# Kernel tuning notes

Hardware: AMD Instinct MI355X
Metric: run time of the kernel (lower is better)

## Reference

```python
import jax, jax.numpy as jnp
import numpy as np

D_MODEL = 1024
N_HEADS = 16
D_HEAD = D_MODEL // N_HEADS
SCALE = D_HEAD ** -0.5


def setup_inputs() -> dict:
    key = jax.random.key(0)
    ks = jax.random.split(key, 9)
    s = 0.02
    x = jax.random.normal(ks[0], (2, 2048, D_MODEL), dtype=jnp.float32)
    Wq = jax.random.normal(ks[1], (D_MODEL, D_MODEL), dtype=jnp.float32) * s
    Wk = jax.random.normal(ks[2], (D_MODEL, D_MODEL), dtype=jnp.float32) * s
    Wv = jax.random.normal(ks[3], (D_MODEL, D_MODEL), dtype=jnp.float32) * s
    Wo = jax.random.normal(ks[4], (D_MODEL, D_MODEL), dtype=jnp.float32) * s
    bq = jax.random.normal(ks[5], (D_MODEL,), dtype=jnp.float32) * s
    bk = jax.random.normal(ks[6], (D_MODEL,), dtype=jnp.float32) * s
    bv = jax.random.normal(ks[7], (D_MODEL,), dtype=jnp.float32) * s
    bo = jax.random.normal(ks[8], (D_MODEL,), dtype=jnp.float32) * s
    return {"x": x, "Wq": Wq, "bq": bq, "Wk": Wk, "bk": bk,
            "Wv": Wv, "bv": bv, "Wo": Wo, "bo": bo}


def reference(x, Wq, bq, Wk, bk, Wv, bv, Wo, bo):
    B, S, _ = x.shape
    # torch nn.Linear: y = x @ W.T + b
    def proj(W, b):
        h = jnp.einsum('bsd,ed->bse', x, W) + b
        return h.reshape(B, S, N_HEADS, D_HEAD).transpose(0, 2, 1, 3)  # [B,H,S,Dh]
    Q = proj(Wq, bq)
    K = proj(Wk, bk)
    V = proj(Wv, bv)
    # chunked QK^T softmax over full K == full attention (no mask, dropout=0)
    scores = jnp.einsum('bhqd,bhkd->bhqk', Q, K) * SCALE  # [B,H,S,S]
    attn = jax.nn.softmax(scores, axis=-1)
    out = jnp.einsum('bhqk,bhkd->bhqd', attn, V)
    out = out.transpose(0, 2, 1, 3).reshape(B, S, D_MODEL)
    return jnp.einsum('bsd,ed->bse', out, Wo) + bo
```

## Files before the change

kernel.cpp:

```cpp
#include <hip/hip_runtime.h>
#include <cstdint>
#include <cstddef>


typedef unsigned short u16;
typedef unsigned int u32;
typedef __bf16 bf16x8 __attribute__((ext_vector_type(8)));
typedef float f32x4 __attribute__((ext_vector_type(4)));

#define GLOAD_LDS16(gp, lp)                                                            \
  __builtin_amdgcn_global_load_lds((const __attribute__((address_space(1))) void*)(gp),\
                                   (__attribute__((address_space(3))) void*)(lp),      \
                                   16, 0, 0)

__device__ __forceinline__ u16 f2bf(float f) {
  unsigned u = __builtin_bit_cast(unsigned, f);
  u = u + 0x7fffu + ((u >> 16) & 1u);
  return (u16)(u >> 16);
}

__device__ __forceinline__ u32 pack_bf2(float a, float b) {
  u32 ua = __builtin_bit_cast(u32, a) + 0x8000u;
  u32 ub = __builtin_bit_cast(u32, b) + 0x8000u;
  return __builtin_amdgcn_perm(ub, ua, 0x07060302u);
}

#define QSCALE 0.1803368801111204f

__global__ void cvt_all(const float* __restrict__ x,
                        const float* __restrict__ wq, const float* __restrict__ wk,
                        const float* __restrict__ wv, const float* __restrict__ wo,
                        u16* __restrict__ xb, u16* __restrict__ wqb,
                        u16* __restrict__ wkb, u16* __restrict__ wvb,
                        u16* __restrict__ wob) {
  int bx = blockIdx.x;
  const float* s; u16* d; int off;
  if (bx < 2048)      { s = x;  d = xb;  off = bx; }
  else if (bx < 2560) { s = wq; d = wqb; off = bx - 2048; }
  else if (bx < 3072) { s = wk; d = wkb; off = bx - 2560; }
  else if (bx < 3584) { s = wv; d = wvb; off = bx - 3072; }
  else                { s = wo; d = wob; off = bx - 3584; }
  int i = off * 2048 + threadIdx.x * 8;
  float4 a = *(const float4*)(s + i);
  float4 b = *(const float4*)(s + i + 4);
  uint4 o;
  o.x = f2bf(a.x) | ((u32)f2bf(a.y) << 16);
  o.y = f2bf(a.z) | ((u32)f2bf(a.w) << 16);
  o.z = f2bf(b.x) | ((u32)f2bf(b.y) << 16);
  o.w = f2bf(b.z) | ((u32)f2bf(b.w) << 16);
  *(uint4*)(d + i) = o;
}

template <int MODE, int BM>
__global__ __launch_bounds__(256, 3) void gemm_mfma(
    const u16* __restrict__ A,
    const u16* __restrict__ W0, const u16* __restrict__ W1, const u16* __restrict__ W2,
    const float* __restrict__ b0, const float* __restrict__ b1, const float* __restrict__ b2,
    u16* __restrict__ o0, u16* __restrict__ o1, u16* __restrict__ o2,
    float* __restrict__ oF)
{
  constexpr int MF = BM / 32;
  constexpr int AG = BM / 32;

  __shared__ __align__(16) u16 As[BM * 64];
  __shared__ __align__(16) u16 Bs[128 * 64];

  const int tid = threadIdx.x;
  const int w = tid >> 6, l = tid & 63;
  const int lane = l & 15, quad = l >> 4;
  const int wm = w >> 1, wn = w & 1;
  const int m0 = blockIdx.y * BM;
  const int n0g = blockIdx.x * 128;

  const int src = (MODE == 0) ? (n0g >> 10) : 0;
  const u16* Wsel = (MODE == 0) ? (src == 0 ? W0 : (src == 1 ? W1 : W2)) : W0;
  const float* bsel = (MODE == 0) ? (src == 0 ? b0 : (src == 1 ? b1 : b2)) : b0;
  const int n_base = (MODE == 0) ? (n0g & 1023) : n0g;

  const int c8 = ((l & 7) ^ (l >> 3)) * 8;
  const int lrow = l >> 3;

  f32x4 acc[MF][4] = {};

  for (int kt = 0; kt < 1024; kt += 64) {
    __syncthreads();
    const u16* Ag = A + (size_t)m0 * 1024 + kt;
    const u16* Bg = Wsel + (size_t)n_base * 1024 + kt;
    #pragma unroll
    for (int i = 0; i < AG; ++i) {
      int rr = w * (8 * AG) + i * 8;
      GLOAD_LDS16(Ag + (size_t)(rr + lrow) * 1024 + c8, As + rr * 64);
    }
    #pragma unroll
    for (int i = 0; i < 4; ++i) {
      int rr = w * 32 + i * 8;
      GLOAD_LDS16(Bg + (size_t)(rr + lrow) * 1024 + c8, Bs + rr * 64);
    }
    __syncthreads();

    bf16x8 af[MF][2], bf[4][2];
    #pragma unroll
    for (int mf = 0; mf < MF; ++mf)
      #pragma unroll
      for (int ks = 0; ks < 2; ++ks)
        af[mf][ks] = *(const bf16x8*)((const char*)As +
            (wm * (BM / 2) + mf * 16 + lane) * 128 + (((ks * 4 + quad) ^ (lane & 7)) * 16));
    #pragma unroll
    for (int nf = 0; nf < 4; ++nf)
      #pragma unroll
      for (int ks = 0; ks < 2; ++ks)
        bf[nf][ks] = *(const bf16x8*)((const char*)Bs +
            (wn * 64 + nf * 16 + lane) * 128 + (((ks * 4 + quad) ^ (lane & 7)) * 16));
    #pragma unroll
    for (int ks = 0; ks < 2; ++ks)
      #pragma unroll
      for (int mf = 0; mf < MF; ++mf)
        #pragma unroll
        for (int nf = 0; nf < 4; ++nf)
          acc[mf][nf] = __builtin_amdgcn_mfma_f32_16x16x32_bf16(
              af[mf][ks], bf[nf][ks], acc[mf][nf], 0, 0, 0);
  }

  float bb[4];
  #pragma unroll
  for (int nf = 0; nf < 4; ++nf) bb[nf] = bsel[n_base + wn * 64 + nf * 16 + lane];

  u16* osel = (MODE == 0) ? (src == 0 ? o0 : (src == 1 ? o1 : o2)) : o0;

  #pragma unroll
  for (int mf = 0; mf < MF; ++mf) {
    int mb = m0 + wm * (BM / 2) + mf * 16 + quad * 4;
    #pragma unroll
    for (int nf = 0; nf < 4; ++nf) {
      int n_l = wn * 64 + nf * 16 + lane;
      if (MODE == 0 && src != 1) {
        float sc = (src == 0) ? QSCALE : 1.0f;
        float v0 = (acc[mf][nf][0] + bb[nf]) * sc;
        float v1 = (acc[mf][nf][1] + bb[nf]) * sc;
        float v2 = (acc[mf][nf][2] + bb[nf]) * sc;
        float v3 = (acc[mf][nf][3] + bb[nf]) * sc;
        int bi = mb >> 11, s = mb & 2047;
        int n_in = n_base + n_l;
        int h = n_in >> 6, dh = n_in & 63;
        uint2 pk = make_uint2(pack_bf2(v0, v1), pack_bf2(v2, v3));
        *(uint2*)(osel + (((size_t)(bi * 16 + h) * 64 + dh) * 2048 + s)) = pk;
      } else {
        #pragma unroll
        for (int r = 0; r < 4; ++r) {
          float v = acc[mf][nf][r] + bb[nf];
          int m = mb + r;
          if (MODE == 0) {
            int bi = m >> 11, s = m & 2047;
            int n_in = n_base + n_l;
            int h = n_in >> 6, dh = n_in & 63;
            osel[(((size_t)(bi * 16 + h) * 2048 + s) << 6) + dh] = f2bf(v);
          } else {
            oF[(size_t)m * 1024 + n0g + n_l] = v;
          }
        }
      }
    }
  }
}

union SMemU {
  struct {
    u16 K[3][64 * 64];
    u16 V[3][64 * 64];
  } m;
  struct {
    float O[4][32 * 64];
    float L[4][32];
  } f;
};

__global__ __launch_bounds__(512, 4) void attn_mfma(
    const u16* __restrict__ Qg_, const u16* __restrict__ Kg_,
    const u16* __restrict__ VTg_, u16* __restrict__ Og)
{
  __shared__ __align__(16) SMemU sm;

  const int tid = threadIdx.x;
  const int w = tid >> 6, l = tid & 63;
  const int lane = l & 15, quad = l >> 4;
  const int g = w >> 1;
  const int kh = w & 1;
  const int bh = blockIdx.y;
  const int q0 = blockIdx.x * 128;

  const u16* QTg = Qg_ + (size_t)bh * 64 * 2048;
  const u16* Kg  = Kg_ + (size_t)bh * 2048 * 64;
  const u16* VTg = VTg_ + (size_t)bh * 64 * 2048;

  const int c8 = ((l & 7) ^ (l >> 3)) * 8;
  const int lrow = l >> 3;
  const int rr = w * 8;

  const int qcol = q0 + g * 32 + lane;
  bf16x8 bq[2][2];
  #pragma unroll
  for (int qf = 0; qf < 2; ++qf)
    #pragma unroll
    for (int ks = 0; ks < 2; ++ks) {
      bf16x8 v;
      #pragma unroll
      for (int j = 0; j < 8; ++j)
        v[j] = __builtin_bit_cast(__bf16,
            QTg[(size_t)(ks * 32 + quad * 8 + j) * 2048 + qcol + qf * 16]);
      bq[qf][ks] = v;
    }

  GLOAD_LDS16(Kg + (size_t)(rr + lrow) * 64 + c8, sm.m.K[0] + rr * 64);
  GLOAD_LDS16(VTg + (size_t)(rr + lrow) * 2048 + c8, sm.m.V[0] + rr * 64);
  GLOAD_LDS16(Kg + (size_t)(64 + rr + lrow) * 64 + c8, sm.m.K[1] + rr * 64);
  GLOAD_LDS16(VTg + (size_t)(rr + lrow) * 2048 + 64 + c8, sm.m.V[1] + rr * 64);

  f32x4 oa[2][4] = {};
  float lsum[2] = {0.f, 0.f};
  int cur = 0;

  for (int kt = 0; kt < 32; ++kt) {
    if (kt < 31) asm volatile("s_waitcnt vmcnt(2)" ::: "memory");
    else         asm volatile("s_waitcnt vmcnt(0)" ::: "memory");
    __builtin_amdgcn_s_barrier();
    asm volatile("" ::: "memory");

    if (kt < 30) {
      int pf = (cur == 0) ? 2 : cur - 1;
      GLOAD_LDS16(Kg + (size_t)((kt + 2) * 64 + rr + lrow) * 64 + c8,
                  sm.m.K[pf] + rr * 64);
      GLOAD_LDS16(VTg + (size_t)(rr + lrow) * 2048 + (kt + 2) * 64 + c8,
                  sm.m.V[pf] + rr * 64);
    }

    f32x4 sa[2][2] = {};
    #pragma unroll
    for (int ks = 0; ks < 2; ++ks) {
      bf16x8 ak[2];
      #pragma unroll
      for (int kf = 0; kf < 2; ++kf)
        ak[kf] = *(const bf16x8*)((const char*)sm.m.K[cur] +
            (kh * 32 + kf * 16 + lane) * 128 + (((ks * 4 + quad) ^ (lane & 7)) * 16));
      #pragma unroll
      for (int kf = 0; kf < 2; ++kf)
        #pragma unroll
        for (int qf = 0; qf < 2; ++qf)
          sa[kf][qf] = __builtin_amdgcn_mfma_f32_16x16x32_bf16(
              ak[kf], bq[qf][ks], sa[kf][qf], 0, 0, 0);
    }

    bf16x8 ap[2];
    #pragma unroll
    for (int qf = 0; qf < 2; ++qf) {
      float x0 = __builtin_amdgcn_exp2f(sa[0][qf][0]);
      float x1 = __builtin_amdgcn_exp2f(sa[0][qf][1]);
      float x2 = __builtin_amdgcn_exp2f(sa[0][qf][2]);
      float x3 = __builtin_amdgcn_exp2f(sa[0][qf][3]);
      float y0 = __builtin_amdgcn_exp2f(sa[1][qf][0]);
      float y1 = __builtin_amdgcn_exp2f(sa[1][qf][1]);
      float y2 = __builtin_amdgcn_exp2f(sa[1][qf][2]);
      float y3 = __builtin_amdgcn_exp2f(sa[1][qf][3]);
      lsum[qf] += ((x0 + x1) + (x2 + x3)) + ((y0 + y1) + (y2 + y3));
      u32 X0 = pack_bf2(x0, x1), X1 = pack_bf2(x2, x3);
      u32 Y0 = pack_bf2(y0, y1), Y1 = pack_bf2(y2, y3);
      asm("v_permlane32_swap_b32 %0, %1" : "+v"(X0), "+v"(Y0));
      asm("v_permlane16_swap_b32 %0, %1" : "+v"(X0), "+v"(Y0));
      asm("v_permlane32_swap_b32 %0, %1" : "+v"(X1), "+v"(Y1));
      asm("v_permlane16_swap_b32 %0, %1" : "+v"(X1), "+v"(Y1));
      uint4 d4 = make_uint4(X0, X1, Y0, Y1);
      ap[qf] = __builtin_bit_cast(bf16x8, d4);
    }

    {
      bf16x8 bv[4];
      #pragma unroll
      for (int df = 0; df < 4; ++df)
        bv[df] = *(const bf16x8*)((const char*)sm.m.V[cur] +
            (df * 16 + lane) * 128 + (((kh * 4 + quad) ^ (lane & 7)) * 16));
      #pragma unroll
      for (int qf = 0; qf < 2; ++qf)
        #pragma unroll
        for (int df = 0; df < 4; ++df)
          oa[qf][df] = __builtin_amdgcn_mfma_f32_16x16x32_bf16(
              ap[qf], bv[df], oa[qf][df], 0, 0, 0);
    }

    cur = (cur == 2) ? 0 : cur + 1;
  }

  #pragma unroll
  for (int qf = 0; qf < 2; ++qf) {
    lsum[qf] += __shfl_xor(lsum[qf], 16);
    lsum[qf] += __shfl_xor(lsum[qf], 32);
  }

  __syncthreads();
  if (kh == 1) {
    #pragma unroll
    for (int qf = 0; qf < 2; ++qf)
      #pragma unroll
      for (int df = 0; df < 4; ++df)
        #pragma unroll
        for (int r = 0; r < 4; ++r)
          sm.f.O[g][(qf * 16 + quad * 4 + r) * 64 + df * 16 + lane] = oa[qf][df][r];
    if (l < 16) {
      sm.f.L[g][l] = lsum[0];
      sm.f.L[g][16 + l] = lsum[1];
    }
  }
  __syncthreads();
  if (kh == 0) {
    const int b = bh >> 4, hh = bh & 15;
    u16* Ob = Og + ((size_t)b * 2048 + q0 + g * 32) * 1024 + hh * 64;
    float ltot[2];
    #pragma unroll
    for (int qf = 0; qf < 2; ++qf)
      ltot[qf] = lsum[qf] + sm.f.L[g][qf * 16 + lane];
    #pragma unroll
    for (int qf = 0; qf < 2; ++qf)
      #pragma unroll
      for (int r = 0; r < 4; ++r) {
        float inv = 1.0f / __shfl(ltot[qf], quad * 4 + r, 16);
        int qrow = qf * 16 + quad * 4 + r;
        #pragma unroll
        for (int df = 0; df < 4; ++df) {
          float v = oa[qf][df][r] + sm.f.O[g][qrow * 64 + df * 16 + lane];
          Ob[(size_t)qrow * 1024 + df * 16 + lane] = f2bf(v * inv);
        }
      }
  }
}

extern "C" void kernel_launch(void* const* d_in, const int* in_sizes, int n_in,
                              void* d_out, int out_size, void* d_ws, size_t ws_size,
                              hipStream_t stream)
{
  (void)in_sizes; (void)n_in; (void)out_size; (void)ws_size;
  const float* x  = (const float*)d_in[0];
  const float* Wq = (const float*)d_in[1];
  const float* bq = (const float*)d_in[2];
  const float* Wk = (const float*)d_in[3];
  const float* bk = (const float*)d_in[4];
  const float* Wv = (const float*)d_in[5];
  const float* bv = (const float*)d_in[6];
  const float* Wo = (const float*)d_in[7];
  const float* bo = (const float*)d_in[8];
  float* y = (float*)d_out;

  const size_t NM = (size_t)4096 * 1024;
  u16* xb  = (u16*)d_ws;
  u16* wqb = xb + NM;
  u16* wkb = wqb + 1024 * 1024;
  u16* wvb = wkb + 1024 * 1024;
  u16* wob = wvb + 1024 * 1024;
  u16* Qb  = wob + 1024 * 1024;
  u16* Kb  = Qb + NM;
  u16* VTb = Kb + NM;
  u16* AOb = VTb + NM;

  cvt_all<<<4096, 256, 0, stream>>>(x, Wq, Wk, Wv, Wo, xb, wqb, wkb, wvb, wob);

  gemm_mfma<0, 128><<<dim3(24, 32), 256, 0, stream>>>(
      xb, wqb, wkb, wvb, bq, bk, bv, Qb, Kb, VTb, nullptr);

  attn_mfma<<<dim3(16, 32), 512, 0, stream>>>(Qb, Kb, VTb, AOb);

  gemm_mfma<1, 64><<<dim3(8, 64), 256, 0, stream>>>(
      AOb, wob, nullptr, nullptr, bo, nullptr, nullptr,
      nullptr, nullptr, nullptr, y);
}
```

Measured before the change: 184.1 us.

## Fuse fp32-to-bf16 conversion into GEMM loads and remap block order for XCD locality

Removes the separate cvt_all conversion kernel. The GEMMs now read fp32 x and weights directly, convert them with v_cvt_pk_bf16_f32 and store the result to LDS through registers instead of global_load_lds. Block indices in the GEMM and attention kernels are remapped so that consecutive blocks in each group of eight go to the same tile region, which is meant to improve L2 locality per XCD. In exchange the GEMMs read twice the bytes per tile and repeat the conversion in every block that shares a tile. The async direct-to-LDS path is lost for fp32 operands, and the hardware cvt may round differently from the old software rounding.

```diff
diff --git a/kernel.cpp b/kernel.cpp
--- a/kernel.cpp
+++ b/kernel.cpp
@@ -19,6 +19,12 @@
   return (u16)(u >> 16);
 }
 
+__device__ __forceinline__ u32 cvtpk(float a, float b) {
+  u32 r;
+  asm("v_cvt_pk_bf16_f32 %0, %1, %2" : "=v"(r) : "v"(a), "v"(b));
+  return r;
+}
+
 __device__ __forceinline__ u32 pack_bf2(float a, float b) {
   u32 ua = __builtin_bit_cast(u32, a) + 0x8000u;
   u32 ub = __builtin_bit_cast(u32, b) + 0x8000u;
@@ -27,40 +33,20 @@
 
 #define QSCALE 0.1803368801111204f
 
-__global__ void cvt_all(const float* __restrict__ x,
-                        const float* __restrict__ wq, const float* __restrict__ wk,
-                        const float* __restrict__ wv, const float* __restrict__ wo,
-                        u16* __restrict__ xb, u16* __restrict__ wqb,
-                        u16* __restrict__ wkb, u16* __restrict__ wvb,
-                        u16* __restrict__ wob) {
-  int bx = blockIdx.x;
-  const float* s; u16* d; int off;
-  if (bx < 2048)      { s = x;  d = xb;  off = bx; }
-  else if (bx < 2560) { s = wq; d = wqb; off = bx - 2048; }
-  else if (bx < 3072) { s = wk; d = wkb; off = bx - 2560; }
-  else if (bx < 3584) { s = wv; d = wvb; off = bx - 3072; }
-  else                { s = wo; d = wob; off = bx - 3584; }
-  int i = off * 2048 + threadIdx.x * 8;
-  float4 a = *(const float4*)(s + i);
-  float4 b = *(const float4*)(s + i + 4);
-  uint4 o;
-  o.x = f2bf(a.x) | ((u32)f2bf(a.y) << 16);
-  o.y = f2bf(a.z) | ((u32)f2bf(a.w) << 16);
-  o.z = f2bf(b.x) | ((u32)f2bf(b.y) << 16);
-  o.w = f2bf(b.z) | ((u32)f2bf(b.w) << 16);
-  *(uint4*)(d + i) = o;
-}
-
 template <int MODE, int BM>
 __global__ __launch_bounds__(256, 3) void gemm_mfma(
-    const u16* __restrict__ A,
-    const u16* __restrict__ W0, const u16* __restrict__ W1, const u16* __restrict__ W2,
-    const float* __restrict__ b0, const float* __restrict__ b1, const float* __restrict__ b2,
+    const float* __restrict__ Af, const u16* __restrict__ Ab,
+    const float* __restrict__ W0, const float* __restrict__ W1,
+    const float* __restrict__ W2,
+    const float* __restrict__ b0, const float* __restrict__ b1,
+    const float* __restrict__ b2,
     u16* __restrict__ o0, u16* __restrict__ o1, u16* __restrict__ o2,
     float* __restrict__ oF)
 {
   constexpr int MF = BM / 32;
   constexpr int AG = BM / 32;
+  constexpr int NY = (MODE == 0) ? 32 : 64;
+  constexpr int TOT = (MODE == 0) ? 24 * 32 : 8 * 64;
 
   __shared__ __align__(16) u16 As[BM * 64];
   __shared__ __align__(16) u16 Bs[128 * 64];
@@ -69,11 +55,14 @@
   const int w = tid >> 6, l = tid & 63;
   const int lane = l & 15, quad = l >> 4;
   const int wm = w >> 1, wn = w & 1;
-  const int m0 = blockIdx.y * BM;
-  const int n0g = blockIdx.x * 128;
+
+  const int idb = blockIdx.y * gridDim.x + blockIdx.x;
+  const int lid = (idb & 7) * (TOT >> 3) + (idb >> 3);
+  const int m0 = (lid % NY) * BM;
+  const int n0g = (lid / NY) * 128;
 
   const int src = (MODE == 0) ? (n0g >> 10) : 0;
-  const u16* Wsel = (MODE == 0) ? (src == 0 ? W0 : (src == 1 ? W1 : W2)) : W0;
+  const float* Wsel = (MODE == 0) ? (src == 0 ? W0 : (src == 1 ? W1 : W2)) : W0;
   const float* bsel = (MODE == 0) ? (src == 0 ? b0 : (src == 1 ? b1 : b2)) : b0;
   const int n_base = (MODE == 0) ? (n0g & 1023) : n0g;
 
@@ -84,17 +73,38 @@
 
   for (int kt = 0; kt < 1024; kt += 64) {
     __syncthreads();
-    const u16* Ag = A + (size_t)m0 * 1024 + kt;
-    const u16* Bg = Wsel + (size_t)n_base * 1024 + kt;
-    #pragma unroll
-    for (int i = 0; i < AG; ++i) {
-      int rr = w * (8 * AG) + i * 8;
-      GLOAD_LDS16(Ag + (size_t)(rr + lrow) * 1024 + c8, As + rr * 64);
-    }
-    #pragma unroll
-    for (int i = 0; i < 4; ++i) {
-      int rr = w * 32 + i * 8;
-      GLOAD_LDS16(Bg + (size_t)(rr + lrow) * 1024 + c8, Bs + rr * 64);
+    if (MODE == 0) {
+      const float* Ag = Af + (size_t)m0 * 1024 + kt;
+      #pragma unroll
+      for (int i = 0; i < AG; ++i) {
+        int rr = w * (8 * AG) + i * 8;
+        const float* s4 = Ag + (size_t)(rr + lrow) * 1024 + c8;
+        float4 a0 = *(const float4*)(s4);
+        float4 a1 = *(const float4*)(s4 + 4);
+        *(uint4*)((char*)As + rr * 128 + l * 16) =
+            make_uint4(cvtpk(a0.x, a0.y), cvtpk(a0.z, a0.w),
+                       cvtpk(a1.x, a1.y), cvtpk(a1.z, a1.w));
+      }
+    } else {
+      const u16* Ag = Ab + (size_t)m0 * 1024 + kt;
+      #pragma unroll
+      for (int i = 0; i < AG; ++i) {
+        int rr = w * (8 * AG) + i * 8;
+        GLOAD_LDS16(Ag + (size_t)(rr + lrow) * 1024 + c8, As + rr * 64);
+      }
+    }
+    {
+      const float* Bg = Wsel + (size_t)n_base * 1024 + kt;
+      #pragma unroll
+      for (int i = 0; i < 4; ++i) {
+        int rr = w * 32 + i * 8;
+        const float* s4 = Bg + (size_t)(rr + lrow) * 1024 + c8;
+        float4 a0 = *(const float4*)(s4);
+        float4 a1 = *(const float4*)(s4 + 4);
+        *(uint4*)((char*)Bs + rr * 128 + l * 16) =
+            make_uint4(cvtpk(a0.x, a0.y), cvtpk(a0.z, a0.w),
+                       cvtpk(a1.x, a1.y), cvtpk(a1.z, a1.w));
+      }
     }
     __syncthreads();
 
@@ -185,8 +195,11 @@
   const int lane = l & 15, quad = l >> 4;
   const int g = w >> 1;
   const int kh = w & 1;
-  const int bh = blockIdx.y;
-  const int q0 = blockIdx.x * 128;
+
+  const int idb = blockIdx.y * 16 + blockIdx.x;
+  const int lid = (idb & 7) * 64 + (idb >> 3);
+  const int bh = lid >> 4;
+  const int q0 = (lid & 15) * 128;
 
   const u16* QTg = Qg_ + (size_t)bh * 64 * 2048;
   const u16* Kg  = Kg_ + (size_t)bh * 2048 * 64;
@@ -348,24 +361,17 @@
   float* y = (float*)d_out;
 
   const size_t NM = (size_t)4096 * 1024;
-  u16* xb  = (u16*)d_ws;
-  u16* wqb = xb + NM;
-  u16* wkb = wqb + 1024 * 1024;
-  u16* wvb = wkb + 1024 * 1024;
-  u16* wob = wvb + 1024 * 1024;
-  u16* Qb  = wob + 1024 * 1024;
+  u16* Qb  = (u16*)d_ws;
   u16* Kb  = Qb + NM;
   u16* VTb = Kb + NM;
   u16* AOb = VTb + NM;
 
-  cvt_all<<<4096, 256, 0, stream>>>(x, Wq, Wk, Wv, Wo, xb, wqb, wkb, wvb, wob);
-
   gemm_mfma<0, 128><<<dim3(24, 32), 256, 0, stream>>>(
-      xb, wqb, wkb, wvb, bq, bk, bv, Qb, Kb, VTb, nullptr);
+      x, nullptr, Wq, Wk, Wv, bq, bk, bv, Qb, Kb, VTb, nullptr);
 
   attn_mfma<<<dim3(16, 32), 512, 0, stream>>>(Qb, Kb, VTb, AOb);
 
   gemm_mfma<1, 64><<<dim3(8, 64), 256, 0, stream>>>(
-      AOb, wob, nullptr, nullptr, bo, nullptr, nullptr,
+      nullptr, AOb, Wo, nullptr, nullptr, bo, nullptr, nullptr,
       nullptr, nullptr, nullptr, y);
 }
```

Measured after the change: 206.3 us. 12.1% more time.

## Remap block IDs for XCD-aware locality and shrink output GEMM tile

Applied to the files above, without the earlier changes.

Block indices in both GEMMs and the attention kernel are remapped so that consecutive blocks dispatched round-robin to each of the 8 XCDs share the same weight columns or the same head, which should improve L2 reuse. The output projection GEMM now uses a 64x64 tile with twice as many blocks and a higher occupancy hint, giving the 256 CUs more parallelism. The smaller tile lowers per-block reuse and adds more redundant A loads.

```diff
diff --git a/kernel.cpp b/kernel.cpp
--- a/kernel.cpp
+++ b/kernel.cpp
@@ -51,8 +51,8 @@
   *(uint4*)(d + i) = o;
 }
 
-template <int MODE, int BM>
-__global__ __launch_bounds__(256, 3) void gemm_mfma(
+template <int MODE, int BM, int BN>
+__global__ __launch_bounds__(256, MODE == 0 ? 3 : 4) void gemm_mfma(
     const u16* __restrict__ A,
     const u16* __restrict__ W0, const u16* __restrict__ W1, const u16* __restrict__ W2,
     const float* __restrict__ b0, const float* __restrict__ b1, const float* __restrict__ b2,
@@ -60,17 +60,24 @@
     float* __restrict__ oF)
 {
   constexpr int MF = BM / 32;
+  constexpr int NF = BN / 32;
   constexpr int AG = BM / 32;
+  constexpr int BG = BN / 32;
+  constexpr int NY = (MODE == 0) ? 32 : 64;
+  constexpr int TOT = (MODE == 0) ? 24 * 32 : 16 * 64;
 
   __shared__ __align__(16) u16 As[BM * 64];
-  __shared__ __align__(16) u16 Bs[128 * 64];
+  __shared__ __align__(16) u16 Bs[BN * 64];
 
   const int tid = threadIdx.x;
   const int w = tid >> 6, l = tid & 63;
   const int lane = l & 15, quad = l >> 4;
   const int wm = w >> 1, wn = w & 1;
-  const int m0 = blockIdx.y * BM;
-  const int n0g = blockIdx.x * 128;
+
+  const int idb = blockIdx.y * gridDim.x + blockIdx.x;
+  const int lid = (idb & 7) * (TOT >> 3) + (idb >> 3);
+  const int m0 = (lid % NY) * BM;
+  const int n0g = (lid / NY) * BN;
 
   const int src = (MODE == 0) ? (n0g >> 10) : 0;
   const u16* Wsel = (MODE == 0) ? (src == 0 ? W0 : (src == 1 ? W1 : W2)) : W0;
@@ -80,7 +87,7 @@
   const int c8 = ((l & 7) ^ (l >> 3)) * 8;
   const int lrow = l >> 3;
 
-  f32x4 acc[MF][4] = {};
+  f32x4 acc[MF][NF] = {};
 
   for (int kt = 0; kt < 1024; kt += 64) {
     __syncthreads();
@@ -92,13 +99,13 @@
       GLOAD_LDS16(Ag + (size_t)(rr + lrow) * 1024 + c8, As + rr * 64);
     }
     #pragma unroll
-    for (int i = 0; i < 4; ++i) {
-      int rr = w * 32 + i * 8;
+    for (int i = 0; i < BG; ++i) {
+      int rr = w * (8 * BG) + i * 8;
       GLOAD_LDS16(Bg + (size_t)(rr + lrow) * 1024 + c8, Bs + rr * 64);
     }
     __syncthreads();
 
-    bf16x8 af[MF][2], bf[4][2];
+    bf16x8 af[MF][2], bf[NF][2];
     #pragma unroll
     for (int mf = 0; mf < MF; ++mf)
       #pragma unroll
@@ -106,24 +113,25 @@
         af[mf][ks] = *(const bf16x8*)((const char*)As +
             (wm * (BM / 2) + mf * 16 + lane) * 128 + (((ks * 4 + quad) ^ (lane & 7)) * 16));
     #pragma unroll
-    for (int nf = 0; nf < 4; ++nf)
+    for (int nf = 0; nf < NF; ++nf)
       #pragma unroll
       for (int ks = 0; ks < 2; ++ks)
         bf[nf][ks] = *(const bf16x8*)((const char*)Bs +
-            (wn * 64 + nf * 16 + lane) * 128 + (((ks * 4 + quad) ^ (lane & 7)) * 16));
+            (wn * (BN / 2) + nf * 16 + lane) * 128 + (((ks * 4 + quad) ^ (lane & 7)) * 16));
     #pragma unroll
     for (int ks = 0; ks < 2; ++ks)
       #pragma unroll
       for (int mf = 0; mf < MF; ++mf)
         #pragma unroll
-        for (int nf = 0; nf < 4; ++nf)
+        for (int nf = 0; nf < NF; ++nf)
           acc[mf][nf] = __builtin_amdgcn_mfma_f32_16x16x32_bf16(
               af[mf][ks], bf[nf][ks], acc[mf][nf], 0, 0, 0);
   }
 
-  float bb[4];
+  float bb[NF];
   #pragma unroll
-  for (int nf = 0; nf < 4; ++nf) bb[nf] = bsel[n_base + wn * 64 + nf * 16 + lane];
+  for (int nf = 0; nf < NF; ++nf)
+    bb[nf] = bsel[n_base + wn * (BN / 2) + nf * 16 + lane];
 
   u16* osel = (MODE == 0) ? (src == 0 ? o0 : (src == 1 ? o1 : o2)) : o0;
 
@@ -131,8 +139,8 @@
   for (int mf = 0; mf < MF; ++mf) {
     int mb = m0 + wm * (BM / 2) + mf * 16 + quad * 4;
     #pragma unroll
-    for (int nf = 0; nf < 4; ++nf) {
-      int n_l = wn * 64 + nf * 16 + lane;
+    for (int nf = 0; nf < NF; ++nf) {
+      int n_l = wn * (BN / 2) + nf * 16 + lane;
       if (MODE == 0 && src != 1) {
         float sc = (src == 0) ? QSCALE : 1.0f;
         float v0 = (acc[mf][nf][0] + bb[nf]) * sc;
@@ -185,8 +193,11 @@
   const int lane = l & 15, quad = l >> 4;
   const int g = w >> 1;
   const int kh = w & 1;
-  const int bh = blockIdx.y;
-  const int q0 = blockIdx.x * 128;
+
+  const int idb = blockIdx.y * 16 + blockIdx.x;
+  const int lid = (idb & 7) * 64 + (idb >> 3);
+  const int bh = lid >> 4;
+  const int q0 = (lid & 15) * 128;
 
   const u16* QTg = Qg_ + (size_t)bh * 64 * 2048;
   const u16* Kg  = Kg_ + (size_t)bh * 2048 * 64;
@@ -360,12 +371,12 @@
 
   cvt_all<<<4096, 256, 0, stream>>>(x, Wq, Wk, Wv, Wo, xb, wqb, wkb, wvb, wob);
 
-  gemm_mfma<0, 128><<<dim3(24, 32), 256, 0, stream>>>(
+  gemm_mfma<0, 128, 128><<<dim3(24, 32), 256, 0, stream>>>(
       xb, wqb, wkb, wvb, bq, bk, bv, Qb, Kb, VTb, nullptr);
 
   attn_mfma<<<dim3(16, 32), 512, 0, stream>>>(Qb, Kb, VTb, AOb);
 
-  gemm_mfma<1, 64><<<dim3(8, 64), 256, 0, stream>>>(
+  gemm_mfma<1, 64, 64><<<dim3(16, 64), 256, 0, stream>>>(
       AOb, wob, nullptr, nullptr, bo, nullptr, nullptr,
       nullptr, nullptr, nullptr, y);
 }
```

New measurement: 178.2 us. 1.03x faster.
